# Optimization experiments

Measured on AMD Instinct MI355X. Metric: run time of the kernel, lower is better.

## Reference

```python
import jax, jax.numpy as jnp
import numpy as np

N, F, H, R, DEG, K = 8192, 64, 128, 3, 32, 32
TEMP = 0.3          # config.edge_temperature
NEG_SLOPE = 0.2     # LeakyReLU slope
EPS_LN = 1e-5
W_THRESH = 1e-6


def setup_inputs() -> dict:
    key = jax.random.key(0)
    ks = jax.random.split(key, 16)
    E = N * DEG
    # each node has DEG outgoing edges so no softmax row is empty (-inf everywhere)
    src = jnp.repeat(jnp.arange(N), DEG)
    tgt = jax.random.randint(ks[0], (E,), 0, N)
    edge_index = jnp.stack([src, tgt]).astype(jnp.int64)
    x = jax.random.normal(ks[1], (N, F), jnp.float32)
    edge_attr = jax.random.normal(ks[2], (E, 3), jnp.float32)
    s = lambda k, sh: jax.random.normal(k, sh, jnp.float32) * 0.05
    D = 2 * F + 3  # edge_input_dim
    params = dict(
        Ws1=s(ks[3], (D, H)), bs1=jnp.zeros(H), ln_g=jnp.ones(H), ln_b=jnp.zeros(H),
        Ws2=s(ks[4], (H, 1)), bs2=jnp.zeros(1),
        Wp=s(ks[5], (D, H)), bp=jnp.zeros(H),
        Wr1=s(ks[6], (F, H)), br1=jnp.zeros(H), Wr2=s(ks[7], (H, R)), br2=jnp.zeros(R),
        Wg1=s(ks[8], (R, H, H // 2)), bg1=jnp.zeros((R, H // 2)),
        Wg2=s(ks[9], (R, H // 2, 1)), bg2=jnp.zeros((R, 1)),
        Wc1=s(ks[10], (F, H)), bc1=jnp.zeros(H), Wc2=s(ks[11], (H, 1)), bc2=jnp.zeros(1),
    )
    return {"x": x, "edge_index": edge_index, "edge_attr": edge_attr, **params}


def reference(x, edge_index, edge_attr,
              Ws1, bs1, ln_g, ln_b, Ws2, bs2, Wp, bp,
              Wr1, br1, Wr2, br2, Wg1, bg1, Wg2, bg2,
              Wc1, bc1, Wc2, bc2):
    src, tgt = edge_index[0], edge_index[1]
    num_nodes = x.shape[0]

    # regime encoder on global mean state
    gs = x.mean(axis=0)
    regime_probs = jax.nn.softmax(jax.nn.relu(gs @ Wr1 + br1) @ Wr2 + br2)  # [R]

    # contagion detector (scalar level)
    contagion_level = jax.nn.sigmoid(jax.nn.relu(x @ Wc1 + bc1) @ Wc2 + bc2).mean()

    # gather -> edge MLP scorer with LayerNorm + LeakyReLU
    edge_input = jnp.concatenate([x[src], x[tgt], edge_attr], axis=-1)  # [E, 2F+3]
    h = edge_input @ Ws1 + bs1
    mu = h.mean(-1, keepdims=True)
    var = h.var(-1, keepdims=True)
    h = (h - mu) * jax.lax.rsqrt(var + EPS_LN) * ln_g + ln_b
    h = jnp.where(h >= 0, h, NEG_SLOPE * h)
    edge_scores_raw = h @ Ws2 + bs2  # [E, 1]

    # regime gating
    edge_hidden = jax.nn.relu(edge_input @ Wp + bp)  # [E, H]
    g1 = jax.nn.relu(jnp.einsum('eh,rhm->erm', edge_hidden, Wg1) + bg1)
    gates = jax.nn.sigmoid(jnp.einsum('erm,rmo->ero', g1, Wg2) + bg2)[..., 0]  # [E, R]
    gate_combined = (gates * regime_probs).sum(-1, keepdims=True)  # [E, 1]

    amp = 1.0 + 0.5 * contagion_level
    edge_scores = (edge_scores_raw * gate_combined * amp)[:, 0]  # [E]

    # scatter into dense NxN, masked softmax per source row, top-k
    M = jnp.full((num_nodes, num_nodes), -jnp.inf, x.dtype).at[src, tgt].set(edge_scores)
    P = jax.nn.softmax(M / TEMP, axis=-1)  # [N, N]
    topk_values, topk_indices = jax.lax.top_k(P, K)  # [N, K]

    # in-device compaction equivalent: weights below threshold zeroed (dropped edges)
    new_edge_weights = jnp.where(topk_values > W_THRESH, topk_values, 0.0)  # [N, K]
    return new_edge_weights, topk_indices
```

## Files before the change

kernel.cpp:

```cpp
#include <hip/hip_runtime.h>
#include <hip/hip_bf16.h>
#include <math.h>

#define NN 8192
#define FF 64
#define HH 128
#define RR 3
#define DEG 32
#define KK 32
#define EE (NN*DEG)
#define DD 131
#define TEMP 0.3f
#define NEG_SLOPE 0.2f
#define EPS_LN 1e-5f
#define W_THRESH 1e-6f

__device__ __forceinline__ float4 ld4(const float* p) { return *(const float4*)p; }


__global__ __launch_bounds__(256) void stats_kernel(
    const float* __restrict__ x, const float* __restrict__ Wc1,
    const float* __restrict__ bc1, const float* __restrict__ Wc2,
    const float* __restrict__ bc2, float* __restrict__ hdr)
{
    __shared__ float xs[64 * 65];
    __shared__ float wl[64 * 128];
    __shared__ float cs[4][64];
    int t = threadIdx.x;
    int n0 = blockIdx.x * 64;

    for (int i = 0; i < 16; i++) {
        int flat = t + i * 256;
        int r = flat >> 6, c = flat & 63;
        xs[r * 65 + c] = x[(n0 + r) * 64 + c];
    }
    for (int i = 0; i < 32; i++) {
        int flat = t + i * 256;
        wl[flat] = Wc1[flat];
    }
    __syncthreads();

    {
        int col = t & 63, g = t >> 6;
        float ps = 0.f;
        for (int r = g * 16; r < g * 16 + 16; r++) ps += xs[r * 65 + col];
        cs[g][col] = ps;
    }
    __syncthreads();
    if (t < 64) {
        float v = cs[0][t] + cs[1][t] + cs[2][t] + cs[3][t];
        atomicAdd(&hdr[8 + t], v);
    }

    int r = t >> 2, q = t & 3;
    float accl = 0.f;
    for (int hh = 0; hh < 32; hh++) {
        int h = hh * 4 + q;
        float s = bc1[h];
        for (int i = 0; i < 64; i++) s += xs[r * 65 + i] * wl[i * 128 + h];
        accl += fmaxf(s, 0.f) * Wc2[h];
    }
    accl += __shfl_xor(accl, 1);
    accl += __shfl_xor(accl, 2);
    if (q == 0) {
        float lvl = 1.f / (1.f + expf(-(accl + bc2[0])));
        atomicAdd(&hdr[0], lvl);
    }
}

__global__ __launch_bounds__(128) void regime_kernel(
    const float* __restrict__ Wr1, const float* __restrict__ br1,
    const float* __restrict__ Wr2, const float* __restrict__ br2,
    float* __restrict__ hdr)
{
    __shared__ float gsl[64];
    __shared__ float t1[128];
    int t = threadIdx.x;
    if (t < 64) gsl[t] = hdr[8 + t] * (1.f / (float)NN);
    __syncthreads();
    float a = br1[t];
    for (int i = 0; i < 64; i++) a += gsl[i] * Wr1[i * 128 + t];
    t1[t] = fmaxf(a, 0.f);
    __syncthreads();
    if (t < 3) {
        float v = br2[t];
        for (int h = 0; h < 128; h++) v += t1[h] * Wr2[h * 3 + t];
        gsl[32 + t] = v;
    }
    __syncthreads();
    if (t == 0) {
        float v0 = gsl[32], v1 = gsl[33], v2 = gsl[34];
        float m = fmaxf(v0, fmaxf(v1, v2));
        float e0 = expf(v0 - m), e1 = expf(v1 - m), e2 = expf(v2 - m);
        float inv = 1.f / (e0 + e1 + e2);
        hdr[1] = e0 * inv; hdr[2] = e1 * inv; hdr[3] = e2 * inv;
        hdr[4] = 1.f + 0.5f * (hdr[0] * (1.f / (float)NN));
    }
}

__global__ __launch_bounds__(256) void partial_kernel(
    const float* __restrict__ x, const float* __restrict__ Ws1,
    const float* __restrict__ Wp, float* __restrict__ PA)
{
    __shared__ float xs[32 * 65];
    __shared__ float wl[64 * 128];
    int t = threadIdx.x;
    int which = blockIdx.x & 1;
    int n0 = (blockIdx.x >> 1) * 32;
    const float* base = which ? Wp : Ws1;

    for (int i = t; i < 2048; i += 256)
        xs[(i >> 6) * 65 + (i & 63)] = x[n0 * 64 + i];
    for (int it = 0; it < 8; it++) {
        int flat = (t + it * 256) * 4;
        *(float4*)&wl[flat] = ld4(&base[flat]);
    }
    __syncthreads();

    int row = t >> 3, colg = t & 7;
    float acc[16];
    #pragma unroll
    for (int j = 0; j < 16; j++) acc[j] = 0.f;
    const float* xr = &xs[row * 65];
    for (int k = 0; k < 64; k++) {
        float a = xr[k];
        const float* wr = &wl[k * 128 + colg * 16];
        #pragma unroll
        for (int jj = 0; jj < 4; jj++) {
            float4 w = ld4(wr + 4 * jj);
            acc[4*jj+0] += a * w.x; acc[4*jj+1] += a * w.y;
            acc[4*jj+2] += a * w.z; acc[4*jj+3] += a * w.w;
        }
    }
    float* outp = PA + (size_t)which * (NN * 128) + (size_t)(n0 + row) * 128 + colg * 16;
    #pragma unroll
    for (int j = 0; j < 16; j++) outp[j] = acc[j];
}

#define EIB_STRIDE 76
#define EHT_STRIDE 68
__global__ __launch_bounds__(256) void edge_score_kernel(
    const int* __restrict__ tgt_idx, const float* __restrict__ edge_attr,
    const float* __restrict__ x,
    const float* __restrict__ Ws1, const float* __restrict__ bs1,
    const float* __restrict__ ln_g, const float* __restrict__ ln_b,
    const float* __restrict__ Ws2, const float* __restrict__ bs2,
    const float* __restrict__ Wp, const float* __restrict__ bp,
    const float* __restrict__ Wg1, const float* __restrict__ bg1,
    const float* __restrict__ Wg2, const float* __restrict__ bg2,
    const float* __restrict__ PA1, const float* __restrict__ PA2,
    const float* __restrict__ hdr, float* __restrict__ scores)
{
    __shared__ float pool[13184];
    float* EIB   = pool;
    float* WPan  = pool + 4864;
    float* ehT   = pool;
    float* WgG   = pool + 8704;
    float* rawS  = pool + 13056;
    float* gateC = pool + 13120;

    int t = threadIdx.x;
    int e0 = blockIdx.x * 64;

    {
        int r = t >> 2, q = t & 3;
        int ge = e0 + r;
        int tg = tgt_idx[ge];
        for (int ii = q; ii < EIB_STRIDE; ii += 4) {
            float v;
            if (ii < 64) v = x[tg * 64 + ii];
            else if (ii < 67) v = edge_attr[ge * 3 + (ii - 64)];
            else v = 0.f;
            EIB[r * EIB_STRIDE + ii] = v;
        }
    }

    int tcol = t & 7, trow = t >> 3;
    const float* EIr0 = &EIB[(2 * trow) * EIB_STRIDE];
    const float* EIr1 = EIr0 + EIB_STRIDE;
    int src0 = (e0 + 2 * trow) >> 5;
    int src1 = (e0 + 2 * trow + 1) >> 5;

    float accs0[16], accs1[16], accp0[16], accp1[16];

    {
        const float* p1a = &PA1[(size_t)src0 * 128 + tcol * 4];
        const float* p1b = &PA1[(size_t)src1 * 128 + tcol * 4];
        const float* p2a = &PA2[(size_t)src0 * 128 + tcol * 4];
        const float* p2b = &PA2[(size_t)src1 * 128 + tcol * 4];
        #pragma unroll
        for (int jj = 0; jj < 4; jj++) {
            float4 v;
            v = ld4(p1a + jj * 32);
            accs0[4*jj+0]=v.x; accs0[4*jj+1]=v.y; accs0[4*jj+2]=v.z; accs0[4*jj+3]=v.w;
            v = ld4(p1b + jj * 32);
            accs1[4*jj+0]=v.x; accs1[4*jj+1]=v.y; accs1[4*jj+2]=v.z; accs1[4*jj+3]=v.w;
            v = ld4(p2a + jj * 32);
            accp0[4*jj+0]=v.x; accp0[4*jj+1]=v.y; accp0[4*jj+2]=v.z; accp0[4*jj+3]=v.w;
            v = ld4(p2b + jj * 32);
            accp1[4*jj+0]=v.x; accp1[4*jj+1]=v.y; accp1[4*jj+2]=v.z; accp1[4*jj+3]=v.w;
        }
    }

    for (int p = 0; p < 3; p++) {
        __syncthreads();
        #pragma unroll
        for (int i = 0; i < 6; i++) {
            int fid = i * 256 + t;
            int mat = (fid >= 768) ? 1 : 0;
            int loc = fid - mat * 768;
            int pr = loc >> 5;
            int pc = (loc & 31) * 4;
            int wrow = 64 + p * 24 + pr;
            const float* Wsrc = mat ? Wp : Ws1;
            float4 w = (wrow < 131) ? ld4(&Wsrc[wrow * 128 + pc])
                                    : make_float4(0.f, 0.f, 0.f, 0.f);
            *(float4*)&WPan[mat * 3072 + pr * 128 + pc] = w;
        }
        __syncthreads();
        for (int kk = 0; kk < 24; kk++) {
            int k = p * 24 + kk;
            float a0 = EIr0[k];
            float a1 = EIr1[k];
            const float* ws = &WPan[kk * 128 + tcol * 4];
            const float* wq = &WPan[3072 + kk * 128 + tcol * 4];
            #pragma unroll
            for (int jj = 0; jj < 4; jj++) {
                float4 w1 = ld4(ws + jj * 32);
                accs0[jj*4+0] += a0 * w1.x; accs0[jj*4+1] += a0 * w1.y;
                accs0[jj*4+2] += a0 * w1.z; accs0[jj*4+3] += a0 * w1.w;
                accs1[jj*4+0] += a1 * w1.x; accs1[jj*4+1] += a1 * w1.y;
                accs1[jj*4+2] += a1 * w1.z; accs1[jj*4+3] += a1 * w1.w;
                float4 w2 = ld4(wq + jj * 32);
                accp0[jj*4+0] += a0 * w2.x; accp0[jj*4+1] += a0 * w2.y;
                accp0[jj*4+2] += a0 * w2.z; accp0[jj*4+3] += a0 * w2.w;
                accp1[jj*4+0] += a1 * w2.x; accp1[jj*4+1] += a1 * w2.y;
                accp1[jj*4+2] += a1 * w2.z; accp1[jj*4+3] += a1 * w2.w;
            }
        }
    }

    {
        float s0 = 0.f, ss0 = 0.f, s1 = 0.f, ss1 = 0.f;
        #pragma unroll
        for (int j = 0; j < 16; j++) {
            int col = tcol * 4 + (j >> 2) * 32 + (j & 3);
            float b = bs1[col];
            accs0[j] += b; accs1[j] += b;
            s0 += accs0[j]; ss0 += accs0[j] * accs0[j];
            s1 += accs1[j]; ss1 += accs1[j] * accs1[j];
        }
        #pragma unroll
        for (int m = 1; m < 8; m <<= 1) {
            s0 += __shfl_xor(s0, m);  ss0 += __shfl_xor(ss0, m);
            s1 += __shfl_xor(s1, m);  ss1 += __shfl_xor(ss1, m);
        }
        float mu0 = s0 * (1.f / 128.f), mu1 = s1 * (1.f / 128.f);
        float var0 = ss0 * (1.f / 128.f) - mu0 * mu0;
        float var1 = ss1 * (1.f / 128.f) - mu1 * mu1;
        float inv0 = 1.f / sqrtf(var0 + EPS_LN);
        float inv1 = 1.f / sqrtf(var1 + EPS_LN);
        float d0 = 0.f, d1 = 0.f;
        #pragma unroll
        for (int j = 0; j < 16; j++) {
            int col = tcol * 4 + (j >> 2) * 32 + (j & 3);
            float g = ln_g[col], bb = ln_b[col], w2 = Ws2[col];
            float y0 = (accs0[j] - mu0) * inv0 * g + bb;
            float y1 = (accs1[j] - mu1) * inv1 * g + bb;
            y0 = (y0 >= 0.f) ? y0 : NEG_SLOPE * y0;
            y1 = (y1 >= 0.f) ? y1 : NEG_SLOPE * y1;
            d0 += y0 * w2; d1 += y1 * w2;
        }
        #pragma unroll
        for (int m = 1; m < 8; m <<= 1) {
            d0 += __shfl_xor(d0, m); d1 += __shfl_xor(d1, m);
        }
        if (tcol == 0) {
            rawS[2 * trow]     = d0 + bs2[0];
            rawS[2 * trow + 1] = d1 + bs2[0];
        }
    }

    __syncthreads();
    #pragma unroll
    for (int j = 0; j < 16; j++) {
        int col = tcol * 4 + (j >> 2) * 32 + (j & 3);
        float b = bp[col];
        ehT[col * EHT_STRIDE + 2 * trow]     = fmaxf(accp0[j] + b, 0.f);
        ehT[col * EHT_STRIDE + 2 * trow + 1] = fmaxf(accp1[j] + b, 0.f);
    }

    {
        int gtr = t >> 4, gtc = t & 15;
        int grow = t >> 2, gq = t & 3;
        float rp0 = hdr[1], rp1 = hdr[2], rp2 = hdr[3];
        float gc = 0.f;
        for (int rr = 0; rr < 3; rr++) {
            float acc[16];
            #pragma unroll
            for (int j = 0; j < 16; j++) acc[j] = 0.f;
            for (int p = 0; p < 2; p++) {
                __syncthreads();
                #pragma unroll
                for (int i = 0; i < 4; i++) {
                    int fid = i * 256 + t;
                    int pr = fid >> 4;
                    int pc = (fid & 15) * 4;
                    *(float4*)&WgG[pr * 64 + pc] =
                        ld4(&Wg1[(size_t)(rr * 128 + p * 64 + pr) * 64 + pc]);
                }
                __syncthreads();
                for (int kk = 0; kk < 64; kk++) {
                    float4 av = ld4(&ehT[(p * 64 + kk) * EHT_STRIDE + 4 * gtr]);
                    float4 bv = ld4(&WgG[kk * 64 + 4 * gtc]);
                    acc[0]  += av.x * bv.x; acc[1]  += av.x * bv.y; acc[2]  += av.x * bv.z; acc[3]  += av.x * bv.w;
                    acc[4]  += av.y * bv.x; acc[5]  += av.y * bv.y; acc[6]  += av.y * bv.z; acc[7]  += av.y * bv.w;
                    acc[8]  += av.z * bv.x; acc[9]  += av.z * bv.y; acc[10] += av.z * bv.z; acc[11] += av.z * bv.w;
                    acc[12] += av.w * bv.x; acc[13] += av.w * bv.y; acc[14] += av.w * bv.z; acc[15] += av.w * bv.w;
                }
            }
            __syncthreads();
            #pragma unroll
            for (int j = 0; j < 4; j++) {
                float b = bg1[rr * 64 + 4 * gtc + j];
                float4 g;
                g.x = fmaxf(acc[0  + j] + b, 0.f);
                g.y = fmaxf(acc[4  + j] + b, 0.f);
                g.z = fmaxf(acc[8  + j] + b, 0.f);
                g.w = fmaxf(acc[12 + j] + b, 0.f);
                *(float4*)&WgG[(4 * gtc + j) * EHT_STRIDE + 4 * gtr] = g;
            }
            __syncthreads();
            float pacc = 0.f;
            #pragma unroll
            for (int j = 0; j < 16; j++) {
                int m = gq * 4 + (j >> 2) * 16 + (j & 3);
                pacc += WgG[m * EHT_STRIDE + grow] * Wg2[rr * 64 + m];
            }
            pacc += __shfl_xor(pacc, 1);
            pacc += __shfl_xor(pacc, 2);
            float gate = 1.f / (1.f + expf(-(pacc + bg2[rr])));
            float rpr = (rr == 0) ? rp0 : ((rr == 1) ? rp1 : rp2);
            gc += gate * rpr;
        }
        if (gq == 0) gateC[grow] = gc;
    }
    __syncthreads();

    if (t < 64) scores[e0 + t] = rawS[t] * gateC[t] * hdr[4];
}

__global__ __launch_bounds__(64) void finalize_kernel(
    const int* __restrict__ tgt_idx, const float* __restrict__ scores,
    float* __restrict__ out_w, float* __restrict__ out_i)
{
    __shared__ int   tl[32];
    __shared__ float pl[32];
    int j = threadIdx.x;
    int row = blockIdx.x;
    bool lane_active = (j < 32);
    int   tg = 0;
    float s  = -INFINITY;
    if (lane_active) {
        tg = tgt_idx[row * 32 + j];
        s  = scores[row * 32 + j];
        tl[j] = tg;
    }
    __syncthreads();

    bool alive = false;
    if (lane_active) {
        alive = true;
        for (int j2 = j + 1; j2 < 32; j2++)
            if (tl[j2] == tg) { alive = false; break; }
    }
    float z = (lane_active && alive) ? s * (1.f / TEMP) : -INFINITY;
    float m = z;
    #pragma unroll
    for (int mm = 1; mm < 64; mm <<= 1) m = fmaxf(m, __shfl_xor(m, mm));
    float p = (lane_active && alive) ? expf(z - m) : 0.f;
    float sum = p;
    #pragma unroll
    for (int mm = 1; mm < 64; mm <<= 1) sum += __shfl_xor(sum, mm);
    p = p / sum;
    if (lane_active) pl[j] = alive ? p : -1.f;
    __syncthreads();

    int rank = 0, dcount = 0;
    for (int j2 = 0; j2 < 32; j2++) {
        float pj = pl[j2];
        if (pj >= 0.f) {
            dcount++;
            if (lane_active && alive) {
                if (pj > p || (pj == p && tl[j2] < tg)) rank++;
            }
        }
    }
    if (lane_active && alive) {
        out_w[row * 32 + rank] = (p > W_THRESH) ? p : 0.f;
        out_i[row * 32 + rank] = (float)tg;
    }
    if (j == 0) {
        int c = 0;
        for (int slot = dcount; slot < 32; slot++) {
            for (;;) {
                bool found = false;
                for (int q = 0; q < 32; q++) if (tl[q] == c) { found = true; break; }
                if (!found) break;
                c++;
            }
            out_w[row * 32 + slot] = 0.f;
            out_i[row * 32 + slot] = (float)c;
            c++;
        }
    }
}

extern "C" void kernel_launch(void* const* d_in, const int* in_sizes, int n_in,
                              void* d_out, int out_size, void* d_ws, size_t ws_size,
                              hipStream_t stream)
{
    const float* x          = (const float*)d_in[0];
    const int*   edge_index = (const int*)  d_in[1];
    const float* edge_attr  = (const float*)d_in[2];
    const float* Ws1 = (const float*)d_in[3];
    const float* bs1 = (const float*)d_in[4];
    const float* ln_g = (const float*)d_in[5];
    const float* ln_b = (const float*)d_in[6];
    const float* Ws2 = (const float*)d_in[7];
    const float* bs2 = (const float*)d_in[8];
    const float* Wp  = (const float*)d_in[9];
    const float* bp  = (const float*)d_in[10];
    const float* Wr1 = (const float*)d_in[11];
    const float* br1 = (const float*)d_in[12];
    const float* Wr2 = (const float*)d_in[13];
    const float* br2 = (const float*)d_in[14];
    const float* Wg1 = (const float*)d_in[15];
    const float* bg1 = (const float*)d_in[16];
    const float* Wg2 = (const float*)d_in[17];
    const float* bg2 = (const float*)d_in[18];
    const float* Wc1 = (const float*)d_in[19];
    const float* bc1 = (const float*)d_in[20];
    const float* Wc2 = (const float*)d_in[21];
    const float* bc2 = (const float*)d_in[22];

    float* hdr    = (float*)d_ws;
    float* scores = hdr + 128;
    float* tabs   = scores + EE;
    const int* tgt = edge_index + EE;

    hipMemsetAsync(d_ws, 0, 512, stream);
    stats_kernel<<<128, 256, 0, stream>>>(x, Wc1, bc1, Wc2, bc2, hdr);
    regime_kernel<<<1, 128, 0, stream>>>(Wr1, br1, Wr2, br2, hdr);
    partial_kernel<<<(NN / 32) * 2, 256, 0, stream>>>(x, Ws1, Wp, tabs);
    edge_score_kernel<<<EE / 64, 256, 0, stream>>>(
        tgt, edge_attr, x, Ws1, bs1, ln_g, ln_b, Ws2, bs2, Wp, bp,
        Wg1, bg1, Wg2, bg2, tabs, tabs + (size_t)NN * 128, hdr, scores);
    finalize_kernel<<<NN, 64, 0, stream>>>(
        tgt, scores, (float*)d_out, (float*)d_out + NN * KK);
}
```

Before: 517.8 us.

## Shrink edge kernel shared memory and fuse regime gate GEMMs into one pass

Shrinks the edge scoring kernel's shared memory pool (13184 to 8000 floats) by using smaller weight panels (12 rows instead of 24) and computing the hidden-layer transpose in two halves. It also adds a launch_bounds occupancy hint. The three regime gate GEMMs are fused into one pass with three register accumulator sets, so each edge-hidden tile is loaded from LDS once instead of three times. Source-partial loads are deduplicated because both edges a thread handles share a source node. Gathering x rows now uses float4 loads. The cost is many more live registers (48 gate accumulators alongside the existing ones), which may cause spills under the launch_bounds cap, plus more barrier rounds.

```diff
diff --git a/kernel.cpp b/kernel.cpp
--- a/kernel.cpp
+++ b/kernel.cpp
@@ -137,9 +137,8 @@
     for (int j = 0; j < 16; j++) outp[j] = acc[j];
 }
 
-#define EIB_STRIDE 76
-#define EHT_STRIDE 68
-__global__ __launch_bounds__(256) void edge_score_kernel(
+#define EIB_S 76
+__global__ __launch_bounds__(256, 5) void edge_fused_kernel(
     const int* __restrict__ tgt_idx, const float* __restrict__ edge_attr,
     const float* __restrict__ x,
     const float* __restrict__ Ws1, const float* __restrict__ bs1,
@@ -151,13 +150,13 @@
     const float* __restrict__ PA1, const float* __restrict__ PA2,
     const float* __restrict__ hdr, float* __restrict__ scores)
 {
-    __shared__ float pool[13184];
+    __shared__ float pool[8000];
     float* EIB   = pool;
     float* WPan  = pool + 4864;
-    float* ehT   = pool;
-    float* WgG   = pool + 8704;
-    float* rawS  = pool + 13056;
-    float* gateC = pool + 13120;
+    float* ehTh  = pool;
+    float* WgPan = pool + 4352;
+    float* Gbuf  = pool;
+    float* rawS  = pool + 7936;
 
     int t = threadIdx.x;
     int e0 = blockIdx.x * 64;
@@ -166,64 +165,69 @@
         int r = t >> 2, q = t & 3;
         int ge = e0 + r;
         int tg = tgt_idx[ge];
-        for (int ii = q; ii < EIB_STRIDE; ii += 4) {
-            float v;
-            if (ii < 64) v = x[tg * 64 + ii];
-            else if (ii < 67) v = edge_attr[ge * 3 + (ii - 64)];
-            else v = 0.f;
-            EIB[r * EIB_STRIDE + ii] = v;
+        #pragma unroll
+        for (int i = 0; i < 4; i++) {
+            int col = q * 16 + 4 * i;
+            *(float4*)&EIB[r * EIB_S + col] = ld4(&x[tg * 64 + col]);
+        }
+        if (q == 0) {
+            float4 v;
+            v.x = edge_attr[(size_t)ge * 3 + 0];
+            v.y = edge_attr[(size_t)ge * 3 + 1];
+            v.z = edge_attr[(size_t)ge * 3 + 2];
+            v.w = 0.f;
+            *(float4*)&EIB[r * EIB_S + 64] = v;
+        } else if (q == 1) {
+            *(float4*)&EIB[r * EIB_S + 68] = make_float4(0.f, 0.f, 0.f, 0.f);
+        } else if (q == 2) {
+            *(float4*)&EIB[r * EIB_S + 72] = make_float4(0.f, 0.f, 0.f, 0.f);
         }
     }
 
     int tcol = t & 7, trow = t >> 3;
-    const float* EIr0 = &EIB[(2 * trow) * EIB_STRIDE];
-    const float* EIr1 = EIr0 + EIB_STRIDE;
-    int src0 = (e0 + 2 * trow) >> 5;
-    int src1 = (e0 + 2 * trow + 1) >> 5;
+    const float* EIr0 = &EIB[(2 * trow) * EIB_S];
+    const float* EIr1 = EIr0 + EIB_S;
+    int src = (e0 + 2 * trow) >> 5;
 
     float accs0[16], accs1[16], accp0[16], accp1[16];
 
     {
-        const float* p1a = &PA1[(size_t)src0 * 128 + tcol * 4];
-        const float* p1b = &PA1[(size_t)src1 * 128 + tcol * 4];
-        const float* p2a = &PA2[(size_t)src0 * 128 + tcol * 4];
-        const float* p2b = &PA2[(size_t)src1 * 128 + tcol * 4];
+        const float* p1 = &PA1[(size_t)src * 128 + tcol * 4];
+        const float* p2 = &PA2[(size_t)src * 128 + tcol * 4];
         #pragma unroll
         for (int jj = 0; jj < 4; jj++) {
             float4 v;
-            v = ld4(p1a + jj * 32);
+            v = ld4(p1 + jj * 32);
             accs0[4*jj+0]=v.x; accs0[4*jj+1]=v.y; accs0[4*jj+2]=v.z; accs0[4*jj+3]=v.w;
-            v = ld4(p1b + jj * 32);
             accs1[4*jj+0]=v.x; accs1[4*jj+1]=v.y; accs1[4*jj+2]=v.z; accs1[4*jj+3]=v.w;
-            v = ld4(p2a + jj * 32);
+            v = ld4(p2 + jj * 32);
             accp0[4*jj+0]=v.x; accp0[4*jj+1]=v.y; accp0[4*jj+2]=v.z; accp0[4*jj+3]=v.w;
-            v = ld4(p2b + jj * 32);
             accp1[4*jj+0]=v.x; accp1[4*jj+1]=v.y; accp1[4*jj+2]=v.z; accp1[4*jj+3]=v.w;
         }
     }
 
-    for (int p = 0; p < 3; p++) {
+    for (int p = 0; p < 6; p++) {
         __syncthreads();
         #pragma unroll
-        for (int i = 0; i < 6; i++) {
+        for (int i = 0; i < 3; i++) {
             int fid = i * 256 + t;
-            int mat = (fid >= 768) ? 1 : 0;
-            int loc = fid - mat * 768;
+            int mat = (fid >= 384) ? 1 : 0;
+            int loc = fid - mat * 384;
             int pr = loc >> 5;
             int pc = (loc & 31) * 4;
-            int wrow = 64 + p * 24 + pr;
+            int wrow = 64 + p * 12 + pr;
             const float* Wsrc = mat ? Wp : Ws1;
             float4 w = (wrow < 131) ? ld4(&Wsrc[wrow * 128 + pc])
                                     : make_float4(0.f, 0.f, 0.f, 0.f);
-            *(float4*)&WPan[mat * 3072 + pr * 128 + pc] = w;
+            *(float4*)&WPan[mat * 1536 + pr * 128 + pc] = w;
         }
         __syncthreads();
-        for (int kk = 0; kk < 24; kk++) {
-            int k = p * 24 + kk;
+        for (int kk = 0; kk < 12; kk++) {
+            int k = p * 12 + kk;
             float a0 = EIr0[k];
             float a1 = EIr1[k];
             const float* ws = &WPan[kk * 128 + tcol * 4];
-            const float* wq = &WPan[3072 + kk * 128 + tcol * 4];
+            const float* wq = &WPan[1536 + kk * 128 + tcol * 4];
             #pragma unroll
             for (int jj = 0; jj < 4; jj++) {
                 float4 w1 = ld4(ws + jj * 32);
@@ -281,73 +285,83 @@
         }
     }
 
-    __syncthreads();
+    int gtr = t >> 4, gtc = t & 15;
+    int grow = t >> 2, gq = t & 3;
+
+    float gacc[3][16];
     #pragma unroll
-    for (int j = 0; j < 16; j++) {
-        int col = tcol * 4 + (j >> 2) * 32 + (j & 3);
-        float b = bp[col];
-        ehT[col * EHT_STRIDE + 2 * trow]     = fmaxf(accp0[j] + b, 0.f);
-        ehT[col * EHT_STRIDE + 2 * trow + 1] = fmaxf(accp1[j] + b, 0.f);
-    }
-
-    {
-        int gtr = t >> 4, gtc = t & 15;
-        int grow = t >> 2, gq = t & 3;
-        float rp0 = hdr[1], rp1 = hdr[2], rp2 = hdr[3];
-        float gc = 0.f;
-        for (int rr = 0; rr < 3; rr++) {
-            float acc[16];
+    for (int rr = 0; rr < 3; rr++)
+        #pragma unroll
+        for (int j = 0; j < 16; j++) gacc[rr][j] = 0.f;
+
+    for (int hf = 0; hf < 2; hf++) {
+        __syncthreads();
+        #pragma unroll
+        for (int j2 = 0; j2 < 8; j2++) {
+            int j = hf * 8 + j2;
+            int col = tcol * 4 + (j >> 2) * 32 + (j & 3);
+            int lc = col - hf * 64;
+            float b = bp[col];
+            ehTh[lc * 68 + 2 * trow]     = fmaxf(accp0[j] + b, 0.f);
+            ehTh[lc * 68 + 2 * trow + 1] = fmaxf(accp1[j] + b, 0.f);
+        }
+        for (int p = 0; p < 4; p++) {
+            __syncthreads();
             #pragma unroll
-            for (int j = 0; j < 16; j++) acc[j] = 0.f;
-            for (int p = 0; p < 2; p++) {
-                __syncthreads();
+            for (int i = 0; i < 3; i++) {
+                int fid = i * 256 + t;
+                int rr = fid >> 8;
+                int loc = fid & 255;
+                int pr = loc >> 4;
+                int pc = (loc & 15) * 4;
+                *(float4*)&WgPan[rr * 1024 + pr * 64 + pc] =
+                    ld4(&Wg1[(size_t)(rr * 128 + hf * 64 + p * 16 + pr) * 64 + pc]);
+            }
+            __syncthreads();
+            for (int kk = 0; kk < 16; kk++) {
+                float4 av = ld4(&ehTh[(p * 16 + kk) * 68 + 4 * gtr]);
                 #pragma unroll
-                for (int i = 0; i < 4; i++) {
-                    int fid = i * 256 + t;
-                    int pr = fid >> 4;
-                    int pc = (fid & 15) * 4;
-                    *(float4*)&WgG[pr * 64 + pc] =
-                        ld4(&Wg1[(size_t)(rr * 128 + p * 64 + pr) * 64 + pc]);
-                }
-                __syncthreads();
-                for (int kk = 0; kk < 64; kk++) {
-                    float4 av = ld4(&ehT[(p * 64 + kk) * EHT_STRIDE + 4 * gtr]);
-                    float4 bv = ld4(&WgG[kk * 64 + 4 * gtc]);
-                    acc[0]  += av.x * bv.x; acc[1]  += av.x * bv.y; acc[2]  += av.x * bv.z; acc[3]  += av.x * bv.w;
-                    acc[4]  += av.y * bv.x; acc[5]  += av.y * bv.y; acc[6]  += av.y * bv.z; acc[7]  += av.y * bv.w;
-                    acc[8]  += av.z * bv.x; acc[9]  += av.z * bv.y; acc[10] += av.z * bv.z; acc[11] += av.z * bv.w;
-                    acc[12] += av.w * bv.x; acc[13] += av.w * bv.y; acc[14] += av.w * bv.z; acc[15] += av.w * bv.w;
+                for (int rr = 0; rr < 3; rr++) {
+                    float4 bv = ld4(&WgPan[rr * 1024 + kk * 64 + 4 * gtc]);
+                    gacc[rr][0]  += av.x * bv.x; gacc[rr][1]  += av.x * bv.y;
+                    gacc[rr][2]  += av.x * bv.z; gacc[rr][3]  += av.x * bv.w;
+                    gacc[rr][4]  += av.y * bv.x; gacc[rr][5]  += av.y * bv.y;
+                    gacc[rr][6]  += av.y * bv.z; gacc[rr][7]  += av.y * bv.w;
+                    gacc[rr][8]  += av.z * bv.x; gacc[rr][9]  += av.z * bv.y;
+                    gacc[rr][10] += av.z * bv.z; gacc[rr][11] += av.z * bv.w;
+                    gacc[rr][12] += av.w * bv.x; gacc[rr][13] += av.w * bv.y;
+                    gacc[rr][14] += av.w * bv.z; gacc[rr][15] += av.w * bv.w;
                 }
             }
-            __syncthreads();
-            #pragma unroll
-            for (int j = 0; j < 4; j++) {
-                float b = bg1[rr * 64 + 4 * gtc + j];
-                float4 g;
-                g.x = fmaxf(acc[0  + j] + b, 0.f);
-                g.y = fmaxf(acc[4  + j] + b, 0.f);
-                g.z = fmaxf(acc[8  + j] + b, 0.f);
-                g.w = fmaxf(acc[12 + j] + b, 0.f);
-                *(float4*)&WgG[(4 * gtc + j) * EHT_STRIDE + 4 * gtr] = g;
-            }
-            __syncthreads();
-            float pacc = 0.f;
-            #pragma unroll
-            for (int j = 0; j < 16; j++) {
-                int m = gq * 4 + (j >> 2) * 16 + (j & 3);
-                pacc += WgG[m * EHT_STRIDE + grow] * Wg2[rr * 64 + m];
-            }
-            pacc += __shfl_xor(pacc, 1);
-            pacc += __shfl_xor(pacc, 2);
-            float gate = 1.f / (1.f + expf(-(pacc + bg2[rr])));
-            float rpr = (rr == 0) ? rp0 : ((rr == 1) ? rp1 : rp2);
-            gc += gate * rpr;
-        }
-        if (gq == 0) gateC[grow] = gc;
-    }
-    __syncthreads();
-
-    if (t < 64) scores[e0 + t] = rawS[t] * gateC[t] * hdr[4];
+        }
+    }
+
+    float gc = 0.f;
+    for (int rr = 0; rr < 3; rr++) {
+        __syncthreads();
+        #pragma unroll
+        for (int j = 0; j < 4; j++) {
+            float b = bg1[rr * 64 + 4 * gtc + j];
+            float4 g;
+            g.x = fmaxf(gacc[rr][0  + j] + b, 0.f);
+            g.y = fmaxf(gacc[rr][4  + j] + b, 0.f);
+            g.z = fmaxf(gacc[rr][8  + j] + b, 0.f);
+            g.w = fmaxf(gacc[rr][12 + j] + b, 0.f);
+            *(float4*)&Gbuf[(4 * gtc + j) * 68 + 4 * gtr] = g;
+        }
+        __syncthreads();
+        float pacc = 0.f;
+        #pragma unroll
+        for (int j = 0; j < 16; j++) {
+            int m = gq * 4 + (j >> 2) * 16 + (j & 3);
+            pacc += Gbuf[m * 68 + grow] * Wg2[rr * 64 + m];
+        }
+        pacc += __shfl_xor(pacc, 1);
+        pacc += __shfl_xor(pacc, 2);
+        float gate = 1.f / (1.f + expf(-(pacc + bg2[rr])));
+        gc += gate * hdr[1 + rr];
+    }
+    if (gq == 0) scores[e0 + grow] = rawS[grow] * gc * hdr[4];
 }
 
 __global__ __launch_bounds__(64) void finalize_kernel(
@@ -453,7 +467,7 @@
     stats_kernel<<<128, 256, 0, stream>>>(x, Wc1, bc1, Wc2, bc2, hdr);
     regime_kernel<<<1, 128, 0, stream>>>(Wr1, br1, Wr2, br2, hdr);
     partial_kernel<<<(NN / 32) * 2, 256, 0, stream>>>(x, Ws1, Wp, tabs);
-    edge_score_kernel<<<EE / 64, 256, 0, stream>>>(
+    edge_fused_kernel<<<EE / 64, 256, 0, stream>>>(
         tgt, edge_attr, x, Ws1, bs1, ln_g, ln_b, Ws2, bs2, Wp, bp,
         Wg1, bg1, Wg2, bg2, tabs, tabs + (size_t)NN * 128, hdr, scores);
     finalize_kernel<<<NN, 64, 0, stream>>>(
```

Result: no change. 520.3 us (+0.5%).
